# Performance work log

Hardware: AMD Instinct MI355X
Metric: run time of the kernel (lower is better)

The kernel has to match this reference:

```python
import jax, jax.numpy as jnp
import numpy as np

IN_SHAPE, OUT_SHAPE = 512, 2048  # folding3 config from BSANet


def _sample_2d(m, n):
    # Faithful port of BSANet.sample_2D: 46x46 grid over [-0.3, 0.3]^2
    xs = np.linspace(-0.3, 0.3, 46)
    pts = np.stack(np.meshgrid(xs, xs))                    # [2, 46, 46]
    ix = np.round(np.linspace(0, 45, m)).astype(int)
    iy = np.round(np.linspace(0, 45, n)).astype(int)
    gx, gy = np.meshgrid(ix, iy)                           # each [n, m]
    return jnp.asarray(pts[:, gx.ravel(), gy.ravel()].T, jnp.float32)  # [m*n, 2]


def _lin(x, W, b):
    # MLP() in the source is Linear followed by ReLU for EVERY layer
    return jax.nn.relu(x @ W + b)


def setup_inputs() -> dict:
    key = jax.random.key(0)
    ks = jax.random.split(key, 20)
    def w(k, i, o):
        return jax.random.normal(k, (i, o), jnp.float32) / np.float32(np.sqrt(i))
    def bvec(k, o):
        return jax.random.normal(k, (o,), jnp.float32) * 0.01
    return {
        "p": jax.random.normal(ks[0], (32, IN_SHAPE, 128), jnp.float32),
        # SelfAttention MLPs (shared by both Up_module calls, as in the source)
        "Wh": w(ks[1], 256, 64),   "bh": bvec(ks[2], 64),
        "Wl": w(ks[3], 256, 64),   "bl": bvec(ks[4], 64),
        "Wg": w(ks[5], 256, 256),  "bg": bvec(ks[6], 256),
        "Wf": w(ks[7], 256, 128),  "bf": bvec(ks[8], 128),
        # M_up: MLP([130, 128])
        "Wup": w(ks[9], 130, 128), "bup": bvec(ks[10], 128),
        # M_down: MLP([512, 256, 128])
        "Wd1": w(ks[11], 512, 256), "bd1": bvec(ks[12], 256),
        "Wd2": w(ks[13], 256, 128), "bd2": bvec(ks[14], 128),
        "m": 64,
        "n": 32,
    }


def reference(p, Wh, bh, Wl, bl, Wg, bg, Wf, bf, Wup, bup, Wd1, bd1, Wd2, bd2, m, n):
    r = OUT_SHAPE // IN_SHAPE                              # 4
    pts = _sample_2d(m, n)                                 # [2048, 2]

    def up(q):                                             # q: [B, 512, 128]
        q = jnp.tile(q, (1, r, 1))                         # [B, 2048, 128] (torch repeat along dim 1)
        grid = jnp.broadcast_to(pts, (q.shape[0],) + pts.shape)
        q2d = _lin(jnp.concatenate([q, grid], -1), Wup, bup)   # [B, 2048, 128]
        qc = jnp.concatenate([q, q2d], -1)                 # [B, 2048, 256]
        h = _lin(qc, Wh, bh)                               # [B, 2048, 64]
        l = _lin(qc, Wl, bl)                               # [B, 2048, 64]
        g = _lin(qc, Wg, bg)                               # [B, 2048, 256]
        attn = jax.nn.softmax(jnp.einsum('bnd,bmd->bnm', l, h), axis=-1)  # [B, 2048, 2048]
        return _lin(qc + jnp.einsum('bnm,bmd->bnd', attn, g), Wf, bf)     # [B, 2048, 128]

    def down(q):                                           # q: [B, 2048, 128]
        q = q.reshape(q.shape[0], IN_SHAPE, r * q.shape[2])  # [B, 512, 512]
        return _lin(_lin(q, Wd1, bd1), Wd2, bd2)           # [B, 512, 128]

    p1 = up(p)
    p2 = up(p - down(p1))
    return p1 + p2
```

## Files before the change

### kernel.cpp

```cpp
#include <hip/hip_runtime.h>
#include <hip/hip_bf16.h>
#include <cmath>

#define NB   32
#define SOUT 2048
#define SIN  512
#define LOG2E 1.4426950408889634f

typedef __attribute__((ext_vector_type(8))) short bhalf8;
typedef __attribute__((ext_vector_type(4))) float f32x4;

__device__ inline ushort f2b(float x) {
  union { float f; unsigned u; } v; v.f = x;
  unsigned r = v.u + 0x7FFFu + ((v.u >> 16) & 1u);
  return (ushort)(r >> 16);
}
__device__ inline float b2f(ushort u) {
  union { unsigned u; float f; } v; v.u = ((unsigned)u) << 16;
  return v.f;
}
__device__ inline unsigned pkt(float lo, float hi) {
  union { float f; unsigned u; } a, b; a.f = lo; b.f = hi;
  return (a.u >> 16) | (b.u & 0xFFFF0000u);
}

__device__ inline void gload16(const void* g, void* l) {
  __builtin_amdgcn_global_load_lds(
      (const __attribute__((address_space(1))) void*)g,
      (__attribute__((address_space(3))) void*)l, 16, 0, 0);
}

__global__ void pts_kernel(const int* __restrict__ mArr, const int* __restrict__ nArr,
                           float* __restrict__ pts) {
  int k = blockIdx.x * blockDim.x + threadIdx.x;
  if (k >= SOUT) return;
  int m = mArr[0], n = nArr[0];
  int b = k % m, a = k / m;
  int ixb = (int)rint(45.0 * (double)b / (double)(m - 1));
  int iya = (int)rint(45.0 * (double)a / (double)(n - 1));
  const float step = 0.6f / 45.0f;
  pts[2 * k + 0] = -0.3f + step * (float)iya;
  pts[2 * k + 1] = -0.3f + step * (float)ixb;
}

__global__ __launch_bounds__(256) void wconv_kernel(
    const float* __restrict__ Wh, const float* __restrict__ Wl,
    const float* __restrict__ Wg, const float* __restrict__ Wf,
    const float* __restrict__ Wd1, const float* __restrict__ Wd2,
    const float* __restrict__ bh, const float* __restrict__ bl,
    const float* __restrict__ bg, const float* __restrict__ Wup,
    const float* __restrict__ bup, const float* __restrict__ pts,
    ushort* __restrict__ dst, float* __restrict__ fbias,
    float* __restrict__ gridterm) {
  const int which = blockIdx.y;
  int idx = blockIdx.x * 256 + threadIdx.x;
  if (which == 6) {
    if (idx < 384)
      fbias[idx] = idx < 64 ? bh[idx] : (idx < 128 ? bl[idx - 64] : bg[idx - 128]);
    return;
  }
  if (which == 7) {
    if (idx < 2048 * 128) {
      int i = idx >> 7, n = idx & 127;
      gridterm[idx] = bup[n] + pts[2 * i] * Wup[128 * 128 + n]
                             + pts[2 * i + 1] * Wup[129 * 128 + n];
    }
    return;
  }
  if (which == 8) {
    if (idx < 16384) {
      int n = idx >> 7, k = idx & 127;
      dst[294912 + n * 128 + k] = f2b(Wup[k * 128 + n]);
    }
    return;
  }
  const float* src; int K, N; long off;
  switch (which) {
    case 0: src = Wh;  K = 256; N = 64;  off = 0;      break;
    case 1: src = Wl;  K = 256; N = 64;  off = 16384;  break;
    case 2: src = Wg;  K = 256; N = 256; off = 32768;  break;
    case 3: src = Wf;  K = 256; N = 128; off = 98304;  break;
    case 4: src = Wd1; K = 512; N = 256; off = 131072; break;
    default:src = Wd2; K = 256; N = 128; off = 262144; break;
  }
  if (idx >= K * N) return;
  int n = idx / K, k = idx - n * K;
  dst[off + idx] = f2b(src[(long)k * N + n]);
}

__global__ __launch_bounds__(256) void pconv_kernel(
    const float* __restrict__ p, ushort* __restrict__ pb,
    ushort* __restrict__ qcb) {
  int idx = blockIdx.x * 256 + threadIdx.x;
  long base = (long)idx * 4;
  int b = (int)(base >> 16);
  int rem = (int)(base & 65535);
  int i = rem >> 7, n = rem & 127;
  float4 v = *(const float4*)(p + base);
  ushort4 u;
  u.x = f2b(v.x); u.y = f2b(v.y); u.z = f2b(v.z); u.w = f2b(v.w);
  *(ushort4*)(pb + base) = u;
#pragma unroll
  for (int j = 0; j < 4; ++j)
    *(ushort4*)(qcb + ((long)b * 2048 + i + 512 * j) * 256 + n) = u;
}

template <int MODE>
__global__ __launch_bounds__(256) void mgemm(
    const ushort* __restrict__ A, const ushort* __restrict__ Wt,
    const float* __restrict__ bias, void* __restrict__ outv,
    void* __restrict__ out2v, const float* __restrict__ aux,
    int M, int N, int K) {
  __shared__ alignas(16) ushort As[128 * 64];
  __shared__ alignas(16) ushort Bs[128 * 64];
  const int tid = threadIdx.x;
  const int w = tid >> 6, lane = tid & 63, g = lane >> 4, c = lane & 15;
  const int wm = w >> 1, wn = w & 1;
  const long row0 = (long)blockIdx.y * 128;
  const int col0 = blockIdx.x * 128;
  const long Astride = (long)K * 2;
  const char* Wb = (const char*)Wt;
  const long abase = (MODE == 6) ? ((row0 >> 11) * 512 + (row0 & 511)) : row0;
  const char* Ab = (const char*)A + abase * Astride;

  f32x4 acc[4][4];
#pragma unroll
  for (int i = 0; i < 4; ++i)
#pragma unroll
    for (int j = 0; j < 4; ++j) acc[i][j] = (f32x4){0.f, 0.f, 0.f, 0.f};

  for (int k0 = 0; k0 < K; k0 += 64) {
#pragma unroll
    for (int it = 0; it < 4; ++it) {
      int o = it * 4096 + tid * 16;
      int row = o >> 7, cb = o & 127;
      gload16(Ab + (long)row * Astride + k0 * 2 + (cb ^ ((row & 7) << 4)),
              (char*)As + o);
    }
#pragma unroll
    for (int it = 0; it < 4; ++it) {
      int o = it * 4096 + tid * 16;
      int row = o >> 7, cb = o & 127;
      gload16(Wb + (long)(col0 + row) * Astride + k0 * 2 + (cb ^ ((row & 7) << 4)),
              (char*)Bs + o);
    }
    __syncthreads();
#pragma unroll
    for (int koff = 0; koff < 2; ++koff) {
      bhalf8 a[4], bfr[4];
#pragma unroll
      for (int mi = 0; mi < 4; ++mi) {
        int row = 64 * wm + 16 * mi + c;
        a[mi] = *(const bhalf8*)((const char*)As + row * 128 +
                                 ((16 * g + 64 * koff) ^ ((row & 7) << 4)));
      }
#pragma unroll
      for (int ni = 0; ni < 4; ++ni) {
        int row = 64 * wn + 16 * ni + c;
        bfr[ni] = *(const bhalf8*)((const char*)Bs + row * 128 +
                                   ((16 * g + 64 * koff) ^ ((row & 7) << 4)));
      }
#pragma unroll
      for (int mi = 0; mi < 4; ++mi)
#pragma unroll
        for (int ni = 0; ni < 4; ++ni)
          acc[mi][ni] = __builtin_amdgcn_mfma_f32_16x16x32_bf16(a[mi], bfr[ni], acc[mi][ni], 0, 0, 0);
    }
    __syncthreads();
  }

#pragma unroll
  for (int ni = 0; ni < 4; ++ni) {
    int n = col0 + 64 * wn + 16 * ni + c;
    float bn = (MODE == 6) ? 0.f : bias[n];
#pragma unroll
    for (int mi = 0; mi < 4; ++mi) {
      long m0 = row0 + 64 * wm + 16 * mi + 4 * g;
      if (MODE == 6) {
        ushort* O = (ushort*)outv;
#pragma unroll
        for (int r = 0; r < 4; ++r) {
          int i2048 = (int)((m0 + r) & 2047);
          float val = fmaxf(acc[mi][ni][r] + aux[i2048 * 128 + n], 0.f);
          O[(m0 + r) * 256 + 128 + n] = f2b(val);
        }
        continue;
      }
      float v[4];
#pragma unroll
      for (int r = 0; r < 4; ++r) v[r] = fmaxf(acc[mi][ni][r] + bn, 0.f);
      if (MODE == 0) {
        ushort* O = (ushort*)outv;
#pragma unroll
        for (int r = 0; r < 4; ++r) O[(m0 + r) * N + n] = f2b(v[r]);
      } else if (MODE == 7) {
        if (col0 == 0) {
          ushort* O = (ushort*)outv;
          float sc = (n >= 64) ? LOG2E : 1.0f;
#pragma unroll
          for (int r = 0; r < 4; ++r) O[(m0 + r) * 128 + n] = f2b(v[r] * sc);
        } else {
          int bb = (int)(m0 >> 11);
          int ml = (int)(m0 & 2047);
          int d = n - 128;
          ushort4 u4;
          u4.x = f2b(v[0]); u4.y = f2b(v[1]); u4.z = f2b(v[2]); u4.w = f2b(v[3]);
          *(ushort4*)((ushort*)out2v + ((long)bb * 256 + d) * 2048 + ml) = u4;
        }
      } else if (MODE == 3) {
        ushort* Opmb = (ushort*)outv;
        ushort* Oqcb = (ushort*)out2v;
#pragma unroll
        for (int r = 0; r < 4; ++r) {
          float val = aux[(m0 + r) * N + n] - v[r];
          ushort uv = f2b(val);
          Opmb[(m0 + r) * 128 + n] = uv;
          long bb = (m0 + r) >> 9;
          int ii = (int)((m0 + r) & 511);
#pragma unroll
          for (int j = 0; j < 4; ++j)
            Oqcb[(bb * 2048 + ii + 512 * j) * 256 + n] = uv;
        }
      } else {
        float* O = (float*)outv;
        const ushort* auxb = (const ushort*)aux;
#pragma unroll
        for (int r = 0; r < 4; ++r)
          O[(m0 + r) * N + n] = v[r] + b2f(auxb[(m0 + r) * N + n]);
      }
    }
  }
}

__global__ __launch_bounds__(256, 2) void attn_kernel(
    const ushort* __restrict__ hl, const ushort* __restrict__ gtm,
    ushort* __restrict__ qcb) {
  __shared__ alignas(16) ushort Ht[2][64 * 64];
  __shared__ alignas(16) ushort Gs[2][256 * 64];

  const int tid = threadIdx.x;
  const int w = tid >> 6, lane = tid & 63, g = lane >> 4, c = lane & 15;
  const int bid = blockIdx.x;
  const int wg = (bid & 7) * 64 + (bid >> 3);
  const int b = wg >> 4, nb = wg & 15;
  const float THR = 11.0f;

  bhalf8 la[2][2];
#pragma unroll
  for (int qg = 0; qg < 2; ++qg) {
    const ushort* lrow = hl + ((long)b * SOUT + nb * 128 + 32 * w + 16 * qg + c) * 128 + 64 + 8 * g;
    la[qg][0] = *(const bhalf8*)(lrow);
    la[qg][1] = *(const bhalf8*)(lrow + 32);
  }

  float mold[2] = {-INFINITY, -INFINITY}, srow[2] = {0.f, 0.f};
  f32x4 oacc[16][2];
#pragma unroll
  for (int t = 0; t < 16; ++t)
#pragma unroll
    for (int qg = 0; qg < 2; ++qg) oacc[t][qg] = (f32x4){0.f, 0.f, 0.f, 0.f};

  const char* hlbase = (const char*)(hl + (long)b * SOUT * 128);
  const char* gtb = (const char*)(gtm + (long)b * 256 * 2048);

  {
#pragma unroll
    for (int it = 0; it < 2; ++it) {
      int o = it * 4096 + tid * 16;
      int row = o >> 7, cb = o & 127;
      gload16(hlbase + row * 256 + (cb ^ ((row & 7) << 4)), (char*)Ht[0] + o);
    }
#pragma unroll
    for (int it = 0; it < 8; ++it) {
      int o = it * 4096 + tid * 16;
      int row = o >> 7, cb = o & 127;
      gload16(gtb + (long)row * 4096 + (cb ^ ((row & 7) << 4)), (char*)Gs[0] + o);
    }
  }
  __syncthreads();

  const int srcA = c + 32 * (g & 1);
  const int srcB = srcA + 16;
  const bool hi = (g >> 1) != 0;

  for (int mb = 0; mb < 32; ++mb) {
    const int buf = mb & 1;

    if (mb < 31) {
#pragma unroll
      for (int it = 0; it < 2; ++it) {
        int o = it * 4096 + tid * 16;
        int row = o >> 7, cb = o & 127;
        gload16(hlbase + ((long)(mb + 1) * 64 + row) * 256 + (cb ^ ((row & 7) << 4)),
                (char*)Ht[buf ^ 1] + o);
      }
#pragma unroll
      for (int it = 0; it < 8; ++it) {
        int o = it * 4096 + tid * 16;
        int row = o >> 7, cb = o & 127;
        gload16(gtb + (long)row * 4096 + (mb + 1) * 128 + (cb ^ ((row & 7) << 4)),
                (char*)Gs[buf ^ 1] + o);
      }
    }

    const char* hcur = (const char*)Ht[buf];
    f32x4 sacc[2][4];
#pragma unroll
    for (int qg = 0; qg < 2; ++qg)
#pragma unroll
      for (int j = 0; j < 4; ++j) sacc[qg][j] = (f32x4){0.f, 0.f, 0.f, 0.f};
#pragma unroll
    for (int j = 0; j < 4; ++j) {
      int row = 16 * j + c;
#pragma unroll
      for (int s = 0; s < 2; ++s) {
        bhalf8 hbf = *(const bhalf8*)(hcur + row * 128 +
                                      ((64 * s + 16 * g) ^ ((c & 7) << 4)));
        sacc[0][j] = __builtin_amdgcn_mfma_f32_16x16x32_bf16(hbf, la[0][s], sacc[0][j], 0, 0, 0);
        sacc[1][j] = __builtin_amdgcn_mfma_f32_16x16x32_bf16(hbf, la[1][s], sacc[1][j], 0, 0, 0);
      }
    }

    bhalf8 pb[2][2];
#pragma unroll
    for (int qg = 0; qg < 2; ++qg) {
      float mloc = sacc[qg][0][0];
#pragma unroll
      for (int j = 0; j < 4; ++j)
#pragma unroll
        for (int r = 0; r < 4; ++r) mloc = fmaxf(mloc, sacc[qg][j][r]);
      mloc = fmaxf(mloc, __shfl_xor(mloc, 16));
      mloc = fmaxf(mloc, __shfl_xor(mloc, 32));
      float mnew = fmaxf(mold[qg], mloc);
      bool keep = (mloc <= mold[qg] + THR);
      float scl = keep ? 1.0f : exp2f(mold[qg] - mnew);
      mold[qg] = keep ? mold[qg] : mnew;

      float psum = 0.f;
#pragma unroll
      for (int j = 0; j < 4; ++j)
#pragma unroll
        for (int r = 0; r < 4; ++r) {
          float e = exp2f(sacc[qg][j][r] - mold[qg]);
          sacc[qg][j][r] = e; psum += e;
        }
      psum += __shfl_xor(psum, 16);
      psum += __shfl_xor(psum, 32);
      srow[qg] = srow[qg] * scl + psum;
      if (!__all(keep)) {
#pragma unroll
        for (int t = 0; t < 16; ++t) {
          oacc[t][qg][0] *= scl; oacc[t][qg][1] *= scl;
          oacc[t][qg][2] *= scl; oacc[t][qg][3] *= scl;
        }
      }

#pragma unroll
      for (int s2 = 0; s2 < 2; ++s2) {
        int j2 = 2 * s2;
        unsigned wA0 = pkt(sacc[qg][j2][0], sacc[qg][j2][1]);
        unsigned wA1 = pkt(sacc[qg][j2][2], sacc[qg][j2][3]);
        unsigned wB0 = pkt(sacc[qg][j2 + 1][0], sacc[qg][j2 + 1][1]);
        unsigned wB1 = pkt(sacc[qg][j2 + 1][2], sacc[qg][j2 + 1][3]);
        unsigned a0A = (unsigned)__shfl((int)wA0, srcA);
        unsigned b0A = (unsigned)__shfl((int)wB0, srcA);
        unsigned a1A = (unsigned)__shfl((int)wA1, srcA);
        unsigned b1A = (unsigned)__shfl((int)wB1, srcA);
        unsigned a0B = (unsigned)__shfl((int)wA0, srcB);
        unsigned b0B = (unsigned)__shfl((int)wB0, srcB);
        unsigned a1B = (unsigned)__shfl((int)wA1, srcB);
        unsigned b1B = (unsigned)__shfl((int)wB1, srcB);
        union { unsigned u[4]; bhalf8 v; } pw;
        pw.u[0] = hi ? b0A : a0A;
        pw.u[1] = hi ? b1A : a1A;
        pw.u[2] = hi ? b0B : a0B;
        pw.u[3] = hi ? b1B : a1B;
        pb[qg][s2] = pw.v;
      }
    }

    const char* gcur = (const char*)Gs[buf];
#pragma unroll
    for (int s2 = 0; s2 < 2; ++s2) {
#pragma unroll
      for (int t = 0; t < 16; ++t) {
        int row = 16 * t + c;
        bhalf8 ga = *(const bhalf8*)(gcur + row * 128 +
                                     ((64 * s2 + 16 * g) ^ ((c & 7) << 4)));
        oacc[t][0] = __builtin_amdgcn_mfma_f32_16x16x32_bf16(ga, pb[0][s2], oacc[t][0], 0, 0, 0);
        oacc[t][1] = __builtin_amdgcn_mfma_f32_16x16x32_bf16(ga, pb[1][s2], oacc[t][1], 0, 0, 0);
      }
    }

    __syncthreads();
  }

#pragma unroll
  for (int qg = 0; qg < 2; ++qg) {
    float inv = 1.0f / srow[qg];
    long qrow = ((long)b * SOUT + nb * 128 + 32 * w + 16 * qg + c) * 256;
#pragma unroll
    for (int t = 0; t < 16; ++t) {
      long addr = qrow + 16 * t + 4 * g;
      ushort4 cur = *(const ushort4*)(qcb + addr);
      cur.x = f2b(b2f(cur.x) + oacc[t][qg][0] * inv);
      cur.y = f2b(b2f(cur.y) + oacc[t][qg][1] * inv);
      cur.z = f2b(b2f(cur.z) + oacc[t][qg][2] * inv);
      cur.w = f2b(b2f(cur.w) + oacc[t][qg][3] * inv);
      *(ushort4*)(qcb + addr) = cur;
    }
  }
}

extern "C" void kernel_launch(void* const* d_in, const int* in_sizes, int n_in,
                              void* d_out, int out_size, void* d_ws, size_t ws_size,
                              hipStream_t stream) {
  (void)in_sizes; (void)n_in; (void)out_size; (void)ws_size;
  const float* p   = (const float*)d_in[0];
  const float* Wh  = (const float*)d_in[1];
  const float* bh  = (const float*)d_in[2];
  const float* Wl  = (const float*)d_in[3];
  const float* bl  = (const float*)d_in[4];
  const float* Wg  = (const float*)d_in[5];
  const float* bg  = (const float*)d_in[6];
  const float* Wf  = (const float*)d_in[7];
  const float* bf  = (const float*)d_in[8];
  const float* Wup = (const float*)d_in[9];
  const float* bup = (const float*)d_in[10];
  const float* Wd1 = (const float*)d_in[11];
  const float* bd1 = (const float*)d_in[12];
  const float* Wd2 = (const float*)d_in[13];
  const float* bd2 = (const float*)d_in[14];
  const int* mArr  = (const int*)d_in[15];
  const int* nArr  = (const int*)d_in[16];
  float* out = (float*)d_out;

  float* ws       = (float*)d_ws;
  float* pts      = ws;
  float* bhlg     = ws + 4096;
  float* gridterm = bhlg + 512;
  ushort* qcb  = (ushort*)(gridterm + 262144);
  ushort* hlb  = qcb + 16777216;
  ushort* gt   = hlb + 8388608;
  ushort* p1b  = gt + 16777216;
  ushort* d1b  = p1b + 8388608;
  ushort* pb   = d1b + 4194304;
  ushort* pmb  = pb + 2097152;
  ushort* wts  = pmb + 2097152;
  ushort* Wft  = wts + 98304;
  ushort* Wd1t = wts + 131072;
  ushort* Wd2t = wts + 262144;
  ushort* Wupt = wts + 294912;

  pts_kernel<<<8, 256, 0, stream>>>(mArr, nArr, pts);
  wconv_kernel<<<dim3(1024, 9), 256, 0, stream>>>(
      Wh, Wl, Wg, Wf, Wd1, Wd2, bh, bl, bg, Wup, bup, pts, wts, bhlg, gridterm);

  pconv_kernel<<<2048, 256, 0, stream>>>(p, pb, qcb);
  mgemm<6><<<dim3(1, 512), 256, 0, stream>>>(pb, Wupt, bhlg, qcb, nullptr, gridterm, 65536, 128, 128);
  mgemm<7><<<dim3(3, 512), 256, 0, stream>>>(qcb, wts, bhlg, hlb, gt, nullptr, 65536, 384, 256);
  attn_kernel<<<512, 256, 0, stream>>>(hlb, gt, qcb);
  mgemm<0><<<dim3(1, 512), 256, 0, stream>>>(qcb, Wft, bf, p1b, nullptr, nullptr, 65536, 128, 256);

  mgemm<0><<<dim3(2, 128), 256, 0, stream>>>(p1b, Wd1t, bd1, d1b, nullptr, nullptr, 16384, 256, 512);
  mgemm<3><<<dim3(1, 128), 256, 0, stream>>>(d1b, Wd2t, bd2, pmb, qcb, p, 16384, 128, 256);

  mgemm<6><<<dim3(1, 512), 256, 0, stream>>>(pmb, Wupt, bhlg, qcb, nullptr, gridterm, 65536, 128, 128);
  mgemm<7><<<dim3(3, 512), 256, 0, stream>>>(qcb, wts, bhlg, hlb, gt, nullptr, 65536, 384, 256);
  attn_kernel<<<512, 256, 0, stream>>>(hlb, gt, qcb);
  mgemm<8><<<dim3(1, 512), 256, 0, stream>>>(qcb, Wft, bf, out, nullptr, (const float*)p1b, 65536, 128, 256);
}
```

Measured before the change: 401.7 us.

## Pre-tile G into MFMA fragment layout and load it directly from global

The projection kernel that writes g now stores it in a layout already arranged as per-lane MFMA A-fragments, so each lane reads 16 contiguous bytes. The attention kernel drops the shared-memory double buffer for G and loads fragments straight from global/L2 into registers, interleaving those loads with the PV MFMAs. This cuts LDS traffic and shared-memory footprint, and may allow more resident waves. The cost is that every wave separately refetches G from global memory with no cross-wave sharing, and register pressure rises from the extra fragment registers.

```diff
diff --git a/kernel.cpp b/kernel.cpp
--- a/kernel.cpp
+++ b/kernel.cpp
@@ -202,10 +202,17 @@
         } else {
           int bb = (int)(m0 >> 11);
           int ml = (int)(m0 & 2047);
+          int mb = ml >> 6;
+          int s2 = (ml >> 5) & 1;
+          int gg = (ml >> 3) & 3;
+          int w8 = ml & 7;
           int d = n - 128;
+          int t = d >> 4, cc = d & 15;
+          long off = (long)bb * 524288 + mb * 16384 + s2 * 8192 + t * 512 +
+                     (gg * 16 + cc) * 8 + w8;
           ushort4 u4;
           u4.x = f2b(v[0]); u4.y = f2b(v[1]); u4.z = f2b(v[2]); u4.w = f2b(v[3]);
-          *(ushort4*)((ushort*)out2v + ((long)bb * 256 + d) * 2048 + ml) = u4;
+          *(ushort4*)((ushort*)out2v + off) = u4;
         }
       } else if (MODE == 3) {
         ushort* Opmb = (ushort*)outv;
@@ -236,7 +243,6 @@
     const ushort* __restrict__ hl, const ushort* __restrict__ gtm,
     ushort* __restrict__ qcb) {
   __shared__ alignas(16) ushort Ht[2][64 * 64];
-  __shared__ alignas(16) ushort Gs[2][256 * 64];
 
   const int tid = threadIdx.x;
   const int w = tid >> 6, lane = tid & 63, g = lane >> 4, c = lane & 15;
@@ -261,21 +267,13 @@
     for (int qg = 0; qg < 2; ++qg) oacc[t][qg] = (f32x4){0.f, 0.f, 0.f, 0.f};
 
   const char* hlbase = (const char*)(hl + (long)b * SOUT * 128);
-  const char* gtb = (const char*)(gtm + (long)b * 256 * 2048);
-
-  {
-#pragma unroll
-    for (int it = 0; it < 2; ++it) {
-      int o = it * 4096 + tid * 16;
-      int row = o >> 7, cb = o & 127;
-      gload16(hlbase + row * 256 + (cb ^ ((row & 7) << 4)), (char*)Ht[0] + o);
-    }
-#pragma unroll
-    for (int it = 0; it < 8; ++it) {
-      int o = it * 4096 + tid * 16;
-      int row = o >> 7, cb = o & 127;
-      gload16(gtb + (long)row * 4096 + (cb ^ ((row & 7) << 4)), (char*)Gs[0] + o);
-    }
+  const ushort* g2base = gtm + (long)b * 524288 + lane * 8;
+
+#pragma unroll
+  for (int it = 0; it < 2; ++it) {
+    int o = it * 4096 + tid * 16;
+    int row = o >> 7, cb = o & 127;
+    gload16(hlbase + row * 256 + (cb ^ ((row & 7) << 4)), (char*)Ht[0] + o);
   }
   __syncthreads();
 
@@ -285,6 +283,7 @@
 
   for (int mb = 0; mb < 32; ++mb) {
     const int buf = mb & 1;
+    const ushort* g2 = g2base + (long)mb * 16384;
 
     if (mb < 31) {
 #pragma unroll
@@ -294,13 +293,6 @@
         gload16(hlbase + ((long)(mb + 1) * 64 + row) * 256 + (cb ^ ((row & 7) << 4)),
                 (char*)Ht[buf ^ 1] + o);
       }
-#pragma unroll
-      for (int it = 0; it < 8; ++it) {
-        int o = it * 4096 + tid * 16;
-        int row = o >> 7, cb = o & 127;
-        gload16(gtb + (long)row * 4096 + (mb + 1) * 128 + (cb ^ ((row & 7) << 4)),
-                (char*)Gs[buf ^ 1] + o);
-      }
     }
 
     const char* hcur = (const char*)Ht[buf];
@@ -320,6 +312,11 @@
         sacc[1][j] = __builtin_amdgcn_mfma_f32_16x16x32_bf16(hbf, la[1][s], sacc[1][j], 0, 0, 0);
       }
     }
+
+    bhalf8 gb[8];
+#pragma unroll
+    for (int t = 0; t < 8; ++t)
+      gb[t] = *(const bhalf8*)(g2 + t * 512);
 
     bhalf8 pb[2][2];
 #pragma unroll
@@ -379,17 +376,35 @@
       }
     }
 
-    const char* gcur = (const char*)Gs[buf];
-#pragma unroll
-    for (int s2 = 0; s2 < 2; ++s2) {
-#pragma unroll
-      for (int t = 0; t < 16; ++t) {
-        int row = 16 * t + c;
-        bhalf8 ga = *(const bhalf8*)(gcur + row * 128 +
-                                     ((64 * s2 + 16 * g) ^ ((c & 7) << 4)));
-        oacc[t][0] = __builtin_amdgcn_mfma_f32_16x16x32_bf16(ga, pb[0][s2], oacc[t][0], 0, 0, 0);
-        oacc[t][1] = __builtin_amdgcn_mfma_f32_16x16x32_bf16(ga, pb[1][s2], oacc[t][1], 0, 0, 0);
-      }
+    bhalf8 gn[8];
+#pragma unroll
+    for (int t = 0; t < 8; ++t)
+      gn[t] = *(const bhalf8*)(g2 + 4096 + t * 512);
+#pragma unroll
+    for (int t = 0; t < 8; ++t) {
+      oacc[t][0] = __builtin_amdgcn_mfma_f32_16x16x32_bf16(gb[t], pb[0][0], oacc[t][0], 0, 0, 0);
+      oacc[t][1] = __builtin_amdgcn_mfma_f32_16x16x32_bf16(gb[t], pb[1][0], oacc[t][1], 0, 0, 0);
+    }
+#pragma unroll
+    for (int t = 0; t < 8; ++t)
+      gb[t] = *(const bhalf8*)(g2 + 8192 + t * 512);
+#pragma unroll
+    for (int t = 0; t < 8; ++t) {
+      oacc[8 + t][0] = __builtin_amdgcn_mfma_f32_16x16x32_bf16(gn[t], pb[0][0], oacc[8 + t][0], 0, 0, 0);
+      oacc[8 + t][1] = __builtin_amdgcn_mfma_f32_16x16x32_bf16(gn[t], pb[1][0], oacc[8 + t][1], 0, 0, 0);
+    }
+#pragma unroll
+    for (int t = 0; t < 8; ++t)
+      gn[t] = *(const bhalf8*)(g2 + 8192 + 4096 + t * 512);
+#pragma unroll
+    for (int t = 0; t < 8; ++t) {
+      oacc[t][0] = __builtin_amdgcn_mfma_f32_16x16x32_bf16(gb[t], pb[0][1], oacc[t][0], 0, 0, 0);
+      oacc[t][1] = __builtin_amdgcn_mfma_f32_16x16x32_bf16(gb[t], pb[1][1], oacc[t][1], 0, 0, 0);
+    }
+#pragma unroll
+    for (int t = 0; t < 8; ++t) {
+      oacc[8 + t][0] = __builtin_amdgcn_mfma_f32_16x16x32_bf16(gn[t], pb[0][1], oacc[8 + t][0], 0, 0, 0);
+      oacc[8 + t][1] = __builtin_amdgcn_mfma_f32_16x16x32_bf16(gn[t], pb[1][1], oacc[8 + t][1], 0, 0, 0);
     }
 
     __syncthreads();
```

Measured after the change: 493.3 us. 22.8% more time.
